# Performance work log

Measured on AMD Instinct MI355X. Metric: run time of the kernel, lower is better.

The kernel has to match this reference:

```python
import jax, jax.numpy as jnp
import numpy as np

B, G, H1, H2, P, A = 8192, 20000, 512, 256, 128, 64


def setup_inputs() -> dict:
    key = jax.random.key(0)
    ks = jax.random.split(key, 9)
    s = lambda k, shape, fan: jax.random.normal(k, shape, jnp.float32) / np.sqrt(fan)
    return {
        "x": jax.random.normal(ks[0], (B, G), jnp.float32),
        "W1": s(ks[1], (H1, G), G),
        "b1": s(ks[2], (H1,), G),
        "W2": s(ks[3], (H2, H1), H1),
        "b2": s(ks[4], (H2,), H1),
        "W3": s(ks[5], (P, H2, A), H2),
        "b3": s(ks[6], (P, A), H2),
        "W4": s(ks[7], (P, A), A),
        "b4": s(ks[8], (P,), A),
    }


def reference(x, W1, b1, W2, b2, W3, b3, W4, b4):
    # shared trunk: two dense layers with ReLU (torch Linear: y = x @ W.T + b)
    h = jax.nn.relu(x @ W1.T + b1)          # [B, 512]
    h = jax.nn.relu(h @ W2.T + b2)          # [B, 256]
    # per-protein heads, batched over the protein dim P (replaces python loop)
    a = jax.nn.relu(jnp.einsum("bh,pha->bpa", h, W3) + b3)  # [B, P, A]
    out = jnp.einsum("bpa,pa->bp", a, W4) + b4               # [B, P]
    return out
```

## Files before the change

kernel.cpp:

```cpp
#include <hip/hip_runtime.h>
#include <hip/hip_bf16.h>
#include <stdint.h>

typedef unsigned short u16;
typedef __attribute__((ext_vector_type(8))) short short8;
typedef __attribute__((ext_vector_type(8))) u16   u16x8;
typedef __attribute__((ext_vector_type(4))) u16   u16x4;
typedef __attribute__((ext_vector_type(4))) float f32x4;

#define B_DIM  8192
#define G_DIM  20000
#define H1_DIM 512
#define H2_DIM 256
#define P_DIM  128
#define A_DIM  64
#define SPLITK 8
#define NKT_ALL 625

union Frag { short8 s; u16x8 u; };

__device__ __forceinline__ u16 f2b(float f) {
  union { __hip_bfloat16 b; u16 u; } c;
  c.b = __float2bfloat16(f);
  return c.u;
}

__device__ __forceinline__ void gld16(const void* g, void* l) {
  __builtin_amdgcn_global_load_lds(
      (const __attribute__((address_space(1))) void*)g,
      (__attribute__((address_space(3))) void*)l, 16, 0, 0);
}

__global__ void k_convert(const float* __restrict__ src, u16* __restrict__ dst, int n4) {
  int i = blockIdx.x * 256 + threadIdx.x;
  if (i >= n4) return;
  f32x4 v = ((const f32x4*)src)[i];
  u16x4 o;
  o[0] = f2b(v[0]); o[1] = f2b(v[1]);
  o[2] = f2b(v[2]); o[3] = f2b(v[3]);
  ((u16x4*)dst)[i] = o;
}

__global__ void k_convert_w1frag(const float* __restrict__ W1, u16* __restrict__ W1f) {
  int ot = blockIdx.x * 256 + threadIdx.x;
  if (ot >= (H1_DIM / 16) * NKT_ALL * 64) return;
  int rowblk = ot / (NKT_ALL * 64);
  int rem    = ot - rowblk * (NKT_ALL * 64);
  int kt     = rem >> 6;
  int lane   = rem & 63;
  int row = rowblk * 16 + (lane & 15);
  int col = kt * 32 + (lane >> 4) * 8;
  const float* src = W1 + (size_t)row * G_DIM + col;
  f32x4 v0 = *(const f32x4*)src;
  f32x4 v1 = *(const f32x4*)(src + 4);
  u16x8 o;
#pragma unroll
  for (int i = 0; i < 4; ++i) { o[i] = f2b(v0[i]); o[i + 4] = f2b(v1[i]); }
  ((u16x8*)W1f)[ot] = o;
}

__global__ void k_transpose_w3(const float* __restrict__ W3, u16* __restrict__ W3T) {
  int idx = blockIdx.x * 256 + threadIdx.x;
  if (idx >= P_DIM * H2_DIM * A_DIM) return;
  int h = idx & (H2_DIM - 1);
  int a = (idx >> 8) & (A_DIM - 1);
  int p = idx >> 14;
  W3T[idx] = f2b(W3[((size_t)p * H2_DIM + h) * A_DIM + a]);
}

__global__ __launch_bounds__(512, 4)
void k_gemm1(const float* __restrict__ X, const u16* __restrict__ W1f,
             float* __restrict__ partial) {
  const int ks = blockIdx.x & 7;
  const int m0 = (blockIdx.x >> 3) * 64;
  const int kt_begin = (ks == 0) ? 0 : (ks * 78 + 1);
  const int nkt = (ks == 0) ? 79 : 78;

  const int tid  = threadIdx.x;
  const int lane = tid & 63;
  const int w    = tid >> 6;
  const int c15 = lane & 15, j4 = lane >> 4;
  const int w4 = w * 4;

  __shared__ u16 lsA[2][64 * 64];

  const int aRow = tid >> 3;
  const int aG   = tid & 7;
  const int aPhysU16 = aRow * 64 + ((aG ^ (aRow & 7)) * 8);
  const float* aSrc0 = X + (size_t)(m0 + aRow) * G_DIM + aG * 8;

  f32x4 zero = {0.f, 0.f, 0.f, 0.f};
  f32x4 acc[4][4];
#pragma unroll
  for (int m = 0; m < 4; ++m)
#pragma unroll
    for (int n = 0; n < 4; ++n) acc[m][n] = zero;

  auto loadB = [&](int kt, Frag* br) {
#pragma unroll
    for (int n = 0; n < 4; ++n)
      br[n].s = *(const short8*)(W1f + ((size_t)((w4 + n) * NKT_ALL + kt) * 64 + lane) * 8);
  };
  f32x4 ar0, ar1;
  auto loadA = [&](int kt) {
    const float* src = aSrc0 + (size_t)kt * 32;
    ar0 = *(const f32x4*)src;
    ar1 = *(const f32x4*)(src + 4);
  };
  auto writeA = [&](int buf) {
    u16x8 o;
#pragma unroll
    for (int i = 0; i < 4; ++i) { o[i] = f2b(ar0[i]); o[i + 4] = f2b(ar1[i]); }
    *(u16x8*)&lsA[buf][aPhysU16] = o;
  };
  auto readAfr = [&](int buf, int half, Frag* afr) {
#pragma unroll
    for (int m = 0; m < 4; ++m) {
      int row = m * 16 + c15;
      int g = half * 4 + j4;
      int phys = g ^ (row & 7);
      afr[m].s = *(const short8*)&lsA[buf][row * 64 + phys * 8];
    }
  };

  Frag bfrE[4], bfrO[4];

  loadA(kt_begin);
  loadB(kt_begin, bfrE);
  writeA(0);
  asm volatile("s_waitcnt lgkmcnt(0)" ::: "memory");
  __builtin_amdgcn_s_barrier();
  __builtin_amdgcn_sched_barrier(0);

  const int nsuper = 39;
  for (int T = 0; T < nsuper; ++T) {
    const int buf = T & 1;
    const int kt0 = kt_begin + 2 * T;
    const int ktN = 2 * (T + 1);
    const int ktNext = kt_begin + ((ktN < nkt) ? ktN : (nkt - 1));

    loadA(ktNext);
    loadB(kt0 + 1, bfrO);

    Frag afr[4];
    readAfr(buf, 0, afr);
#pragma unroll
    for (int m = 0; m < 4; ++m)
#pragma unroll
      for (int n = 0; n < 4; ++n)
        acc[m][n] = __builtin_amdgcn_mfma_f32_16x16x32_bf16(afr[m].s, bfrE[n].s, acc[m][n], 0, 0, 0);

    loadB(ktNext, bfrE);

    readAfr(buf, 1, afr);
#pragma unroll
    for (int m = 0; m < 4; ++m)
#pragma unroll
      for (int n = 0; n < 4; ++n)
        acc[m][n] = __builtin_amdgcn_mfma_f32_16x16x32_bf16(afr[m].s, bfrO[n].s, acc[m][n], 0, 0, 0);

    writeA(buf ^ 1);
    asm volatile("s_waitcnt lgkmcnt(0)" ::: "memory");
    __builtin_amdgcn_s_barrier();
    __builtin_amdgcn_sched_barrier(0);
  }

  if (nkt == 79) {
    Frag afr[4];
    readAfr(1, 0, afr);
#pragma unroll
    for (int m = 0; m < 4; ++m)
#pragma unroll
      for (int n = 0; n < 4; ++n)
        acc[m][n] = __builtin_amdgcn_mfma_f32_16x16x32_bf16(afr[m].s, bfrE[n].s, acc[m][n], 0, 0, 0);
  }

  float* outp = partial + ((size_t)ks * B_DIM + m0) * H1_DIM;
#pragma unroll
  for (int m = 0; m < 4; ++m)
#pragma unroll
    for (int n = 0; n < 4; ++n)
#pragma unroll
      for (int r = 0; r < 4; ++r) {
        int row = m * 16 + j4 * 4 + r;
        int col = w * 64 + n * 16 + c15;
        outp[(size_t)row * H1_DIM + col] = acc[m][n][r];
      }
}

__global__ void k_reduce1(const float* __restrict__ partial, const float* __restrict__ b1,
                          u16* __restrict__ h1b) {
  const int n4 = B_DIM * H1_DIM / 4;
  int i = blockIdx.x * 256 + threadIdx.x;
  if (i >= n4) return;
  f32x4 s = ((const f32x4*)partial)[i];
#pragma unroll
  for (int k = 1; k < SPLITK; ++k) {
    f32x4 v = ((const f32x4*)partial)[(size_t)k * n4 + i];
    s[0] += v[0]; s[1] += v[1]; s[2] += v[2]; s[3] += v[3];
  }
  f32x4 bb = ((const f32x4*)b1)[i & (H1_DIM / 4 - 1)];
  u16x4 o;
#pragma unroll
  for (int j = 0; j < 4; ++j)
    o[j] = f2b(fmaxf(s[j] + bb[j], 0.f));
  ((u16x4*)h1b)[i] = o;
}

__global__ __launch_bounds__(256, 2)
void k_gemm2(const u16* __restrict__ h1b, const u16* __restrict__ W2b,
             const float* __restrict__ b2, u16* __restrict__ h2b) {
  const int m0 = blockIdx.x * 128;
  const int n0 = blockIdx.y * 64;
  const int tid  = threadIdx.x;
  const int lane = tid & 63;
  const int wid  = tid >> 6;
  const int wr = wid >> 1, wc = wid & 1;
  const int c15 = lane & 15, j4 = lane >> 4;

  __shared__ u16 lsA[2][128 * 32];
  __shared__ u16 lsB[2][64 * 32];

  f32x4 zero = {0.f, 0.f, 0.f, 0.f};
  f32x4 acc[4][2];
#pragma unroll
  for (int m = 0; m < 4; ++m) { acc[m][0] = zero; acc[m][1] = zero; }

  auto stage = [&](int buf, int kt) {
    const int k0 = kt * 32;
#pragma unroll
    for (int c = 0; c < 2; ++c) {
      int lin = c * 256 + tid;
      int row = lin >> 2, slot = lin & 3;
      int gslot = slot ^ ((row >> 1) & 3);
      gld16(h1b + (size_t)(m0 + row) * H1_DIM + k0 + gslot * 8, &lsA[buf][lin * 8]);
    }
    {
      int lin = tid;
      int row = lin >> 2, slot = lin & 3;
      int gslot = slot ^ ((row >> 1) & 3);
      gld16(W2b + (size_t)(n0 + row) * H1_DIM + k0 + gslot * 8, &lsB[buf][lin * 8]);
    }
  };

  stage(0, 0);
  __syncthreads();
  int buf = 0;
  const int nkt = H1_DIM / 32;
  for (int t = 0; t < nkt; ++t) {
    if (t + 1 < nkt) stage(buf ^ 1, t + 1);
    Frag bfr[2];
#pragma unroll
    for (int n = 0; n < 2; ++n) {
      int row = wc * 32 + n * 16 + c15;
      int slot = j4 ^ ((row >> 1) & 3);
      bfr[n].s = *(const short8*)&lsB[buf][row * 32 + slot * 8];
    }
    Frag afr[4];
#pragma unroll
    for (int m = 0; m < 4; ++m) {
      int row = wr * 64 + m * 16 + c15;
      int slot = j4 ^ ((row >> 1) & 3);
      afr[m].s = *(const short8*)&lsA[buf][row * 32 + slot * 8];
    }
#pragma unroll
    for (int m = 0; m < 4; ++m)
#pragma unroll
      for (int n = 0; n < 2; ++n)
        acc[m][n] = __builtin_amdgcn_mfma_f32_16x16x32_bf16(afr[m].s, bfr[n].s, acc[m][n], 0, 0, 0);
    __syncthreads();
    buf ^= 1;
  }

  float b2v[2];
  b2v[0] = b2[n0 + wc * 32 + c15];
  b2v[1] = b2[n0 + wc * 32 + 16 + c15];
#pragma unroll
  for (int m = 0; m < 4; ++m)
#pragma unroll
    for (int n = 0; n < 2; ++n)
#pragma unroll
      for (int r = 0; r < 4; ++r) {
        int row = m0 + wr * 64 + m * 16 + j4 * 4 + r;
        int col = n0 + wc * 32 + n * 16 + c15;
        h2b[(size_t)row * H2_DIM + col] = f2b(fmaxf(acc[m][n][r] + b2v[n], 0.f));
      }
}

__global__ __launch_bounds__(256, 2)
void k_heads(const u16* __restrict__ h2b, const u16* __restrict__ W3T,
             const float* __restrict__ b3, const float* __restrict__ W4,
             const float* __restrict__ b4, float* __restrict__ out) {
  const int m0 = blockIdx.x * 128;
  const int p0 = blockIdx.y * 2;
  const int tid  = threadIdx.x;
  const int lane = tid & 63;
  const int wid  = tid >> 6;
  const int wr = wid >> 1, wc = wid & 1;
  const int c15 = lane & 15, j4 = lane >> 4;

  __shared__ u16 lsA[2][128 * 64];
  __shared__ u16 lsB[2][128 * 64];

  f32x4 zero = {0.f, 0.f, 0.f, 0.f};
  f32x4 acc[4][4];
#pragma unroll
  for (int m = 0; m < 4; ++m)
#pragma unroll
    for (int n = 0; n < 4; ++n) acc[m][n] = zero;

  auto stage = [&](int buf, int kt) {
    const int k0 = kt * 64;
#pragma unroll
    for (int c = 0; c < 4; ++c) {
      int lin = c * 256 + tid;
      int row = lin >> 3, slot = lin & 7;
      int gslot = slot ^ (row & 7);
      gld16(h2b + (size_t)(m0 + row) * H2_DIM + k0 + gslot * 8, &lsA[buf][lin * 8]);
    }
#pragma unroll
    for (int c = 0; c < 4; ++c) {
      int lin = c * 256 + tid;
      int row = lin >> 3, slot = lin & 7;
      int gslot = slot ^ (row & 7);
      gld16(W3T + ((size_t)(p0 * 64 + row)) * H2_DIM + k0 + gslot * 8, &lsB[buf][lin * 8]);
    }
  };

  stage(0, 0);
  __syncthreads();
  int buf = 0;
  const int nkt = H2_DIM / 64;
  for (int t = 0; t < nkt; ++t) {
    if (t + 1 < nkt) stage(buf ^ 1, t + 1);
#pragma unroll
    for (int kk = 0; kk < 2; ++kk) {
      Frag bfr[4];
#pragma unroll
      for (int n = 0; n < 4; ++n) {
        int row = wc * 64 + n * 16 + c15;
        int slot = (kk * 4 + j4) ^ (row & 7);
        bfr[n].s = *(const short8*)&lsB[buf][row * 64 + slot * 8];
      }
      Frag afr[4];
#pragma unroll
      for (int m = 0; m < 4; ++m) {
        int row = wr * 64 + m * 16 + c15;
        int slot = (kk * 4 + j4) ^ (row & 7);
        afr[m].s = *(const short8*)&lsA[buf][row * 64 + slot * 8];
      }
#pragma unroll
      for (int m = 0; m < 4; ++m)
#pragma unroll
        for (int n = 0; n < 4; ++n)
          acc[m][n] = __builtin_amdgcn_mfma_f32_16x16x32_bf16(afr[m].s, bfr[n].s, acc[m][n], 0, 0, 0);
    }
    __syncthreads();
    buf ^= 1;
  }

  const int p = p0 + wc;
  float w4v[4], b3v[4];
#pragma unroll
  for (int n = 0; n < 4; ++n) {
    w4v[n] = W4[p * A_DIM + n * 16 + c15];
    b3v[n] = b3[p * A_DIM + n * 16 + c15];
  }
  const float b4v = b4[p];

  float s[4][4];
#pragma unroll
  for (int m = 0; m < 4; ++m)
#pragma unroll
    for (int r = 0; r < 4; ++r) s[m][r] = 0.f;
#pragma unroll
  for (int m = 0; m < 4; ++m)
#pragma unroll
    for (int n = 0; n < 4; ++n)
#pragma unroll
      for (int r = 0; r < 4; ++r) {
        float v = fmaxf(acc[m][n][r] + b3v[n], 0.f);
        s[m][r] += v * w4v[n];
      }
#pragma unroll
  for (int m = 0; m < 4; ++m)
#pragma unroll
    for (int r = 0; r < 4; ++r) {
      float v = s[m][r];
      v += __shfl_xor(v, 1);
      v += __shfl_xor(v, 2);
      v += __shfl_xor(v, 4);
      v += __shfl_xor(v, 8);
      s[m][r] = v;
    }
  if (c15 == 0) {
#pragma unroll
    for (int m = 0; m < 4; ++m)
#pragma unroll
      for (int r = 0; r < 4; ++r) {
        int row = m0 + wr * 64 + m * 16 + j4 * 4 + r;
        out[(size_t)row * P_DIM + p] = s[m][r] + b4v;
      }
  }
}

extern "C" void kernel_launch(void* const* d_in, const int* in_sizes, int n_in,
                              void* d_out, int out_size, void* d_ws, size_t ws_size,
                              hipStream_t stream) {
  const float* x  = (const float*)d_in[0];
  const float* W1 = (const float*)d_in[1];
  const float* b1 = (const float*)d_in[2];
  const float* W2 = (const float*)d_in[3];
  const float* b2 = (const float*)d_in[4];
  const float* W3 = (const float*)d_in[5];
  const float* b3 = (const float*)d_in[6];
  const float* W4 = (const float*)d_in[7];
  const float* b4 = (const float*)d_in[8];
  float* out = (float*)d_out;

  char* ws = (char*)d_ws;
  u16*   W1f  = (u16*)(ws);
  u16*   W2b  = (u16*)(ws + 20480000);
  u16*   W3T  = (u16*)(ws + 20742144);
  u16*   h1b  = (u16*)(ws + 24936448);
  u16*   h2b  = (u16*)(ws + 33325056);
  float* part = (float*)(ws + 37519360);

  k_convert_w1frag<<<dim3((1280000 + 255) / 256), dim3(256), 0, stream>>>(W1, W1f);
  k_convert<<<dim3(131072 / 4 / 256), dim3(256), 0, stream>>>(W2, W2b, 131072 / 4);
  k_transpose_w3<<<dim3(2097152 / 256), dim3(256), 0, stream>>>(W3, W3T);

  k_gemm1<<<dim3(128 * SPLITK), dim3(512), 0, stream>>>(x, W1f, part);
  k_reduce1<<<dim3(B_DIM * H1_DIM / 4 / 256), dim3(256), 0, stream>>>(part, b1, h1b);
  k_gemm2<<<dim3(64, 4), dim3(256), 0, stream>>>(h1b, W2b, b2, h2b);
  k_heads<<<dim3(64, 64), dim3(256), 0, stream>>>(h2b, W3T, b3, W4, b4, out);
}
```

Before: 373.2 us.

## Pre-pack W3 into MFMA fragment layout and stage full h2 tile once in heads

W3 is now converted into a per-lane MFMA fragment layout, so the heads kernel loads B fragments directly from global memory and no longer stages them through LDS. Each block loads a full 128x256 h2 tile into LDS once and loops over 16 proteins, with 8 waves each handling one protein and half the rows. This removes repeated h2 staging across protein blocks and the double-buffer synchronisation. In exchange it uses 64KB of LDS per block, which may limit occupancy, and relies on cache-served global loads for W3.

```diff
diff --git a/kernel.cpp b/kernel.cpp
--- a/kernel.cpp
+++ b/kernel.cpp
@@ -59,13 +59,21 @@
   ((u16x8*)W1f)[ot] = o;
 }
 
-__global__ void k_transpose_w3(const float* __restrict__ W3, u16* __restrict__ W3T) {
-  int idx = blockIdx.x * 256 + threadIdx.x;
-  if (idx >= P_DIM * H2_DIM * A_DIM) return;
-  int h = idx & (H2_DIM - 1);
-  int a = (idx >> 8) & (A_DIM - 1);
-  int p = idx >> 14;
-  W3T[idx] = f2b(W3[((size_t)p * H2_DIM + h) * A_DIM + a]);
+__global__ void k_convert_w3frag(const float* __restrict__ W3, u16* __restrict__ W3f) {
+  int ot = blockIdx.x * 256 + threadIdx.x;
+  if (ot >= P_DIM * 4 * 8 * 64) return;
+  int p    = ot >> 11;
+  int rem  = ot & 2047;
+  int nf   = rem >> 9;
+  int kt   = (rem >> 6) & 7;
+  int lane = ot & 63;
+  int a  = nf * 16 + (lane & 15);
+  int h0 = kt * 32 + (lane >> 4) * 8;
+  u16x8 o;
+#pragma unroll
+  for (int j = 0; j < 8; ++j)
+    o[j] = f2b(W3[((size_t)p * H2_DIM + h0 + j) * A_DIM + a]);
+  ((u16x8*)W3f)[ot] = o;
 }
 
 __global__ __launch_bounds__(512, 4)
@@ -287,120 +295,106 @@
       }
 }
 
-__global__ __launch_bounds__(256, 2)
-void k_heads(const u16* __restrict__ h2b, const u16* __restrict__ W3T,
+__global__ __launch_bounds__(512, 4)
+void k_heads(const u16* __restrict__ h2b, const u16* __restrict__ W3f,
              const float* __restrict__ b3, const float* __restrict__ W4,
              const float* __restrict__ b4, float* __restrict__ out) {
-  const int m0 = blockIdx.x * 128;
-  const int p0 = blockIdx.y * 2;
+  const int pg = blockIdx.x & 7;
+  const int mb = blockIdx.x >> 3;
+  const int m0 = mb * 128;
+
   const int tid  = threadIdx.x;
   const int lane = tid & 63;
-  const int wid  = tid >> 6;
-  const int wr = wid >> 1, wc = wid & 1;
+  const int w    = tid >> 6;
+  const int mh = w & 1;
+  const int hs = w >> 1;
   const int c15 = lane & 15, j4 = lane >> 4;
 
-  __shared__ u16 lsA[2][128 * 64];
-  __shared__ u16 lsB[2][128 * 64];
+  __shared__ u16 lsA[128 * 256];
+
+#pragma unroll
+  for (int c = 0; c < 8; ++c) {
+    int lin = c * 512 + tid;
+    int row = lin >> 5, slot = lin & 31;
+    int gslot = slot ^ (row & 7);
+    gld16(h2b + (size_t)(m0 + row) * H2_DIM + gslot * 8, (u16*)lsA + lin * 8);
+  }
+  __syncthreads();
 
   f32x4 zero = {0.f, 0.f, 0.f, 0.f};
-  f32x4 acc[4][4];
-#pragma unroll
-  for (int m = 0; m < 4; ++m)
-#pragma unroll
-    for (int n = 0; n < 4; ++n) acc[m][n] = zero;
-
-  auto stage = [&](int buf, int kt) {
-    const int k0 = kt * 64;
-#pragma unroll
-    for (int c = 0; c < 4; ++c) {
-      int lin = c * 256 + tid;
-      int row = lin >> 3, slot = lin & 7;
-      int gslot = slot ^ (row & 7);
-      gld16(h2b + (size_t)(m0 + row) * H2_DIM + k0 + gslot * 8, &lsA[buf][lin * 8]);
-    }
-#pragma unroll
-    for (int c = 0; c < 4; ++c) {
-      int lin = c * 256 + tid;
-      int row = lin >> 3, slot = lin & 7;
-      int gslot = slot ^ (row & 7);
-      gld16(W3T + ((size_t)(p0 * 64 + row)) * H2_DIM + k0 + gslot * 8, &lsB[buf][lin * 8]);
-    }
-  };
-
-  stage(0, 0);
-  __syncthreads();
-  int buf = 0;
-  const int nkt = H2_DIM / 64;
-  for (int t = 0; t < nkt; ++t) {
-    if (t + 1 < nkt) stage(buf ^ 1, t + 1);
-#pragma unroll
-    for (int kk = 0; kk < 2; ++kk) {
+
+  for (int chunk = 0; chunk < 4; ++chunk) {
+    const int p = pg * 16 + chunk * 4 + hs;
+
+    f32x4 acc[4][4];
+#pragma unroll
+    for (int m = 0; m < 4; ++m)
+#pragma unroll
+      for (int n = 0; n < 4; ++n) acc[m][n] = zero;
+
+#pragma unroll
+    for (int kt = 0; kt < 8; ++kt) {
       Frag bfr[4];
 #pragma unroll
-      for (int n = 0; n < 4; ++n) {
-        int row = wc * 64 + n * 16 + c15;
-        int slot = (kk * 4 + j4) ^ (row & 7);
-        bfr[n].s = *(const short8*)&lsB[buf][row * 64 + slot * 8];
+      for (int nf = 0; nf < 4; ++nf)
+        bfr[nf].s = *(const short8*)(W3f + (((size_t)(p * 4 + nf) * 8 + kt) * 64 + lane) * 8);
+      Frag afr[4];
+#pragma unroll
+      for (int mf = 0; mf < 4; ++mf) {
+        int row = mh * 64 + mf * 16 + c15;
+        int g = kt * 4 + j4;
+        int phys = g ^ (row & 7);
+        afr[mf].s = *(const short8*)&lsA[row * 256 + phys * 8];
       }
-      Frag afr[4];
-#pragma unroll
-      for (int m = 0; m < 4; ++m) {
-        int row = wr * 64 + m * 16 + c15;
-        int slot = (kk * 4 + j4) ^ (row & 7);
-        afr[m].s = *(const short8*)&lsA[buf][row * 64 + slot * 8];
+#pragma unroll
+      for (int mf = 0; mf < 4; ++mf)
+#pragma unroll
+        for (int nf = 0; nf < 4; ++nf)
+          acc[mf][nf] = __builtin_amdgcn_mfma_f32_16x16x32_bf16(afr[mf].s, bfr[nf].s, acc[mf][nf], 0, 0, 0);
+    }
+
+    float w4v[4], b3v[4];
+#pragma unroll
+    for (int nf = 0; nf < 4; ++nf) {
+      w4v[nf] = W4[p * A_DIM + nf * 16 + c15];
+      b3v[nf] = b3[p * A_DIM + nf * 16 + c15];
+    }
+    const float b4v = b4[p];
+
+    float s[4][4];
+#pragma unroll
+    for (int mf = 0; mf < 4; ++mf)
+#pragma unroll
+      for (int r = 0; r < 4; ++r) s[mf][r] = 0.f;
+#pragma unroll
+    for (int mf = 0; mf < 4; ++mf)
+#pragma unroll
+      for (int nf = 0; nf < 4; ++nf)
+#pragma unroll
+        for (int r = 0; r < 4; ++r) {
+          float v = fmaxf(acc[mf][nf][r] + b3v[nf], 0.f);
+          s[mf][r] += v * w4v[nf];
+        }
+#pragma unroll
+    for (int mf = 0; mf < 4; ++mf)
+#pragma unroll
+      for (int r = 0; r < 4; ++r) {
+        float v = s[mf][r];
+        v += __shfl_xor(v, 1);
+        v += __shfl_xor(v, 2);
+        v += __shfl_xor(v, 4);
+        v += __shfl_xor(v, 8);
+        s[mf][r] = v;
       }
-#pragma unroll
-      for (int m = 0; m < 4; ++m)
-#pragma unroll
-        for (int n = 0; n < 4; ++n)
-          acc[m][n] = __builtin_amdgcn_mfma_f32_16x16x32_bf16(afr[m].s, bfr[n].s, acc[m][n], 0, 0, 0);
-    }
-    __syncthreads();
-    buf ^= 1;
-  }
-
-  const int p = p0 + wc;
-  float w4v[4], b3v[4];
-#pragma unroll
-  for (int n = 0; n < 4; ++n) {
-    w4v[n] = W4[p * A_DIM + n * 16 + c15];
-    b3v[n] = b3[p * A_DIM + n * 16 + c15];
-  }
-  const float b4v = b4[p];
-
-  float s[4][4];
-#pragma unroll
-  for (int m = 0; m < 4; ++m)
-#pragma unroll
-    for (int r = 0; r < 4; ++r) s[m][r] = 0.f;
-#pragma unroll
-  for (int m = 0; m < 4; ++m)
-#pragma unroll
-    for (int n = 0; n < 4; ++n)
-#pragma unroll
-      for (int r = 0; r < 4; ++r) {
-        float v = fmaxf(acc[m][n][r] + b3v[n], 0.f);
-        s[m][r] += v * w4v[n];
-      }
-#pragma unroll
-  for (int m = 0; m < 4; ++m)
-#pragma unroll
-    for (int r = 0; r < 4; ++r) {
-      float v = s[m][r];
-      v += __shfl_xor(v, 1);
-      v += __shfl_xor(v, 2);
-      v += __shfl_xor(v, 4);
-      v += __shfl_xor(v, 8);
-      s[m][r] = v;
-    }
-  if (c15 == 0) {
-#pragma unroll
-    for (int m = 0; m < 4; ++m)
-#pragma unroll
-      for (int r = 0; r < 4; ++r) {
-        int row = m0 + wr * 64 + m * 16 + j4 * 4 + r;
-        out[(size_t)row * P_DIM + p] = s[m][r] + b4v;
-      }
+    if (c15 == 0) {
+#pragma unroll
+      for (int mf = 0; mf < 4; ++mf)
+#pragma unroll
+        for (int r = 0; r < 4; ++r) {
+          int row = m0 + mh * 64 + mf * 16 + j4 * 4 + r;
+          out[(size_t)row * P_DIM + p] = s[mf][r] + b4v;
+        }
+    }
   }
 }
 
@@ -421,17 +415,17 @@
   char* ws = (char*)d_ws;
   u16*   W1f  = (u16*)(ws);
   u16*   W2b  = (u16*)(ws + 20480000);
-  u16*   W3T  = (u16*)(ws + 20742144);
+  u16*   W3f  = (u16*)(ws + 20742144);
   u16*   h1b  = (u16*)(ws + 24936448);
   u16*   h2b  = (u16*)(ws + 33325056);
   float* part = (float*)(ws + 37519360);
 
   k_convert_w1frag<<<dim3((1280000 + 255) / 256), dim3(256), 0, stream>>>(W1, W1f);
   k_convert<<<dim3(131072 / 4 / 256), dim3(256), 0, stream>>>(W2, W2b, 131072 / 4);
-  k_transpose_w3<<<dim3(2097152 / 256), dim3(256), 0, stream>>>(W3, W3T);
+  k_convert_w3frag<<<dim3(262144 / 256), dim3(256), 0, stream>>>(W3, W3f);
 
   k_gemm1<<<dim3(128 * SPLITK), dim3(512), 0, stream>>>(x, W1f, part);
   k_reduce1<<<dim3(B_DIM * H1_DIM / 4 / 256), dim3(256), 0, stream>>>(part, b1, h1b);
   k_gemm2<<<dim3(64, 4), dim3(256), 0, stream>>>(h1b, W2b, b2, h2b);
-  k_heads<<<dim3(64, 64), dim3(256), 0, stream>>>(h2b, W3T, b3, W4, b4, out);
-}
+  k_heads<<<dim3(512), dim3(512), 0, stream>>>(h2b, W3f, b3, W4, b4, out);
+}
```

Result: slower. 455.3 us (+22.0%).

## Retile gemm1 to 32-row blocks with 4 waves each covering 128 columns

Applied to the files above, without the earlier changes.

Changes the first GEMM block tile from 64 rows × 512 cols with 8 waves to 32 rows × 512 cols with 4 waves, each wave computing 2×8 MFMA tiles. The grid doubles and shared memory per block halves, aiming for more blocks in flight. It also drops the explicit double-buffered B-fragment register prefetch and the manual waitcnt/sched_barrier scheme in favour of plain __syncthreads and in-loop B loads. The cost is that every W1 fragment is now read from global memory by twice as many blocks, and B load latency is less hidden.

```diff
diff --git a/kernel.cpp b/kernel.cpp
--- a/kernel.cpp
+++ b/kernel.cpp
@@ -68,11 +68,11 @@
   W3T[idx] = f2b(W3[((size_t)p * H2_DIM + h) * A_DIM + a]);
 }
 
-__global__ __launch_bounds__(512, 4)
+__global__ __launch_bounds__(256, 3)
 void k_gemm1(const float* __restrict__ X, const u16* __restrict__ W1f,
              float* __restrict__ partial) {
   const int ks = blockIdx.x & 7;
-  const int m0 = (blockIdx.x >> 3) * 64;
+  const int m0 = (blockIdx.x >> 3) * 32;
   const int kt_begin = (ks == 0) ? 0 : (ks * 78 + 1);
   const int nkt = (ks == 0) ? 79 : 78;
 
@@ -80,9 +80,9 @@
   const int lane = tid & 63;
   const int w    = tid >> 6;
   const int c15 = lane & 15, j4 = lane >> 4;
-  const int w4 = w * 4;
-
-  __shared__ u16 lsA[2][64 * 64];
+  const int w8 = w * 8;
+
+  __shared__ u16 lsA[2][32 * 64];
 
   const int aRow = tid >> 3;
   const int aG   = tid & 7;
@@ -90,17 +90,12 @@
   const float* aSrc0 = X + (size_t)(m0 + aRow) * G_DIM + aG * 8;
 
   f32x4 zero = {0.f, 0.f, 0.f, 0.f};
-  f32x4 acc[4][4];
-#pragma unroll
-  for (int m = 0; m < 4; ++m)
-#pragma unroll
-    for (int n = 0; n < 4; ++n) acc[m][n] = zero;
-
-  auto loadB = [&](int kt, Frag* br) {
-#pragma unroll
-    for (int n = 0; n < 4; ++n)
-      br[n].s = *(const short8*)(W1f + ((size_t)((w4 + n) * NKT_ALL + kt) * 64 + lane) * 8);
-  };
+  f32x4 acc[2][8];
+#pragma unroll
+  for (int m = 0; m < 2; ++m)
+#pragma unroll
+    for (int n = 0; n < 8; ++n) acc[m][n] = zero;
+
   f32x4 ar0, ar1;
   auto loadA = [&](int kt) {
     const float* src = aSrc0 + (size_t)kt * 32;
@@ -113,24 +108,10 @@
     for (int i = 0; i < 4; ++i) { o[i] = f2b(ar0[i]); o[i + 4] = f2b(ar1[i]); }
     *(u16x8*)&lsA[buf][aPhysU16] = o;
   };
-  auto readAfr = [&](int buf, int half, Frag* afr) {
-#pragma unroll
-    for (int m = 0; m < 4; ++m) {
-      int row = m * 16 + c15;
-      int g = half * 4 + j4;
-      int phys = g ^ (row & 7);
-      afr[m].s = *(const short8*)&lsA[buf][row * 64 + phys * 8];
-    }
-  };
-
-  Frag bfrE[4], bfrO[4];
 
   loadA(kt_begin);
-  loadB(kt_begin, bfrE);
   writeA(0);
-  asm volatile("s_waitcnt lgkmcnt(0)" ::: "memory");
-  __builtin_amdgcn_s_barrier();
-  __builtin_amdgcn_sched_barrier(0);
+  __syncthreads();
 
   const int nsuper = 39;
   for (int T = 0; T < nsuper; ++T) {
@@ -140,50 +121,62 @@
     const int ktNext = kt_begin + ((ktN < nkt) ? ktN : (nkt - 1));
 
     loadA(ktNext);
-    loadB(kt0 + 1, bfrO);
-
-    Frag afr[4];
-    readAfr(buf, 0, afr);
-#pragma unroll
-    for (int m = 0; m < 4; ++m)
-#pragma unroll
-      for (int n = 0; n < 4; ++n)
-        acc[m][n] = __builtin_amdgcn_mfma_f32_16x16x32_bf16(afr[m].s, bfrE[n].s, acc[m][n], 0, 0, 0);
-
-    loadB(ktNext, bfrE);
-
-    readAfr(buf, 1, afr);
-#pragma unroll
-    for (int m = 0; m < 4; ++m)
-#pragma unroll
-      for (int n = 0; n < 4; ++n)
-        acc[m][n] = __builtin_amdgcn_mfma_f32_16x16x32_bf16(afr[m].s, bfrO[n].s, acc[m][n], 0, 0, 0);
+
+#pragma unroll
+    for (int half = 0; half < 2; ++half) {
+      const int kt = kt0 + half;
+      Frag bfr[8];
+#pragma unroll
+      for (int n = 0; n < 8; ++n)
+        bfr[n].s = *(const short8*)(W1f + ((size_t)((w8 + n) * NKT_ALL + kt) * 64 + lane) * 8);
+      Frag afr[2];
+#pragma unroll
+      for (int m = 0; m < 2; ++m) {
+        int row = m * 16 + c15;
+        int g = half * 4 + j4;
+        int phys = g ^ (row & 7);
+        afr[m].s = *(const short8*)&lsA[buf][row * 64 + phys * 8];
+      }
+#pragma unroll
+      for (int m = 0; m < 2; ++m)
+#pragma unroll
+        for (int n = 0; n < 8; ++n)
+          acc[m][n] = __builtin_amdgcn_mfma_f32_16x16x32_bf16(afr[m].s, bfr[n].s, acc[m][n], 0, 0, 0);
+    }
 
     writeA(buf ^ 1);
-    asm volatile("s_waitcnt lgkmcnt(0)" ::: "memory");
-    __builtin_amdgcn_s_barrier();
-    __builtin_amdgcn_sched_barrier(0);
+    __syncthreads();
   }
 
   if (nkt == 79) {
-    Frag afr[4];
-    readAfr(1, 0, afr);
-#pragma unroll
-    for (int m = 0; m < 4; ++m)
-#pragma unroll
-      for (int n = 0; n < 4; ++n)
-        acc[m][n] = __builtin_amdgcn_mfma_f32_16x16x32_bf16(afr[m].s, bfrE[n].s, acc[m][n], 0, 0, 0);
+    const int kt = kt_begin + 78;
+    Frag bfr[8];
+#pragma unroll
+    for (int n = 0; n < 8; ++n)
+      bfr[n].s = *(const short8*)(W1f + ((size_t)((w8 + n) * NKT_ALL + kt) * 64 + lane) * 8);
+    Frag afr[2];
+#pragma unroll
+    for (int m = 0; m < 2; ++m) {
+      int row = m * 16 + c15;
+      int phys = j4 ^ (row & 7);
+      afr[m].s = *(const short8*)&lsA[1][row * 64 + phys * 8];
+    }
+#pragma unroll
+    for (int m = 0; m < 2; ++m)
+#pragma unroll
+      for (int n = 0; n < 8; ++n)
+        acc[m][n] = __builtin_amdgcn_mfma_f32_16x16x32_bf16(afr[m].s, bfr[n].s, acc[m][n], 0, 0, 0);
   }
 
   float* outp = partial + ((size_t)ks * B_DIM + m0) * H1_DIM;
 #pragma unroll
-  for (int m = 0; m < 4; ++m)
-#pragma unroll
-    for (int n = 0; n < 4; ++n)
+  for (int m = 0; m < 2; ++m)
+#pragma unroll
+    for (int n = 0; n < 8; ++n)
 #pragma unroll
       for (int r = 0; r < 4; ++r) {
         int row = m * 16 + j4 * 4 + r;
-        int col = w * 64 + n * 16 + c15;
+        int col = w * 128 + n * 16 + c15;
         outp[(size_t)row * H1_DIM + col] = acc[m][n][r];
       }
 }
@@ -430,7 +423,7 @@
   k_convert<<<dim3(131072 / 4 / 256), dim3(256), 0, stream>>>(W2, W2b, 131072 / 4);
   k_transpose_w3<<<dim3(2097152 / 256), dim3(256), 0, stream>>>(W3, W3T);
 
-  k_gemm1<<<dim3(128 * SPLITK), dim3(512), 0, stream>>>(x, W1f, part);
+  k_gemm1<<<dim3(256 * SPLITK), dim3(256), 0, stream>>>(x, W1f, part);
   k_reduce1<<<dim3(B_DIM * H1_DIM / 4 / 256), dim3(256), 0, stream>>>(part, b1, h1b);
   k_gemm2<<<dim3(64, 4), dim3(256), 0, stream>>>(h1b, W2b, b2, h2b);
   k_heads<<<dim3(64, 64), dim3(256), 0, stream>>>(h2b, W3T, b3, W4, b4, out);
```

Measured after the change: 451.1 us. 1.21x slower.
